# Kernel optimization log

Measured on AMD Instinct MI355X. Metric: run time of the kernel, lower is better.

## Reference

```python
import jax, jax.numpy as jnp
import numpy as np

INF = jnp.float32(1e9)


def _hungarian_min_perm(Cp, n):
    """Shortest-augmenting-path Hungarian (e-maxx variant) on padded cost Cp.
    Cp: (n+1, n+1) with Cp[i, j] = C[i-1, j-1] for i,j >= 1; row/col 0 virtual.
    Returns p: (n+1,) int32 where p[j] (j>=1) is the 1-based row assigned to col j.
    """
    cols = jnp.arange(n + 1)

    def outer(i, carry):
        u, v, p = carry
        p = p.at[0].set(i)
        init = (jnp.int32(0), u, v, p,
                jnp.full(n + 1, INF, Cp.dtype),
                jnp.zeros(n + 1, bool),
                jnp.zeros(n + 1, jnp.int32))

        def cond(s):
            j0, u, v, p, minv, used, way = s
            return p[j0] != 0

        def body(s):
            j0, u, v, p, minv, used, way = s
            used = used.at[j0].set(True)
            i0 = p[j0]
            cur = Cp[i0] - u[i0] - v                      # reduced costs, (n+1,)
            avail = (~used) & (cols >= 1)
            better = avail & (cur < minv)
            minv = jnp.where(better, cur, minv)
            way = jnp.where(better, j0, way)
            mv = jnp.where(avail, minv, INF)
            j1 = jnp.argmin(mv).astype(jnp.int32)
            delta = mv[j1]
            u = u.at[p].add(jnp.where(used, delta, 0.0))  # u[p[j]] += delta for used j
            v = v - jnp.where(used, delta, 0.0)
            minv = jnp.where(used, minv, minv - delta)
            return (j1, u, v, p, minv, used, way)

        j0, u, v, p, minv, used, way = jax.lax.while_loop(cond, body, init)

        # reconstruct augmenting path
        def cond2(s):
            return s[0] != 0

        def body2(s):
            j0, p = s
            j1 = way[j0]
            return (j1, p.at[j0].set(p[j1]))

        _, p = jax.lax.while_loop(cond2, body2, (j0, p))
        return (u, v, p)

    u0 = jnp.zeros(n + 1, Cp.dtype)
    v0 = jnp.zeros(n + 1, Cp.dtype)
    p0 = jnp.zeros(n + 1, jnp.int32)
    _, _, p = jax.lax.fori_loop(1, n + 1, outer, (u0, v0, p0))
    return p


def hungarian_maximize(a):
    """a: (n, n) benefit matrix -> (n, n) 0/1 optimal assignment matrix (maximize)."""
    n = a.shape[0]
    Cp = jnp.zeros((n + 1, n + 1), a.dtype).at[1:, 1:].set(-a)  # minimize -a
    p = _hungarian_min_perm(Cp, n)
    return jnp.zeros((n, n), jnp.float32).at[p[1:] - 1, jnp.arange(n)].set(1.0)


batched_lsa = jax.vmap(hungarian_maximize)


def setup_inputs() -> dict:
    key = jax.random.key(0)
    B, H, W = 1024, 128, 128
    x = jax.random.normal(key, (B, H, W), dtype=jnp.float32)
    bias = jnp.ones((H, W), dtype=jnp.float32)  # nn.Parameter(torch.ones(h, w))
    return {"x": x, "bias": bias}


def reference(x, bias):
    perm = batched_lsa(x)                               # (B, h, w) 0/1 assignments
    out = perm / jnp.sqrt(jnp.sum(perm * perm))         # global L2 norm (dim=None, keepdim)
    out = out * bias                                    # broadcast (h, w)
    return jax.nn.softmax(out, axis=2)                  # w >= h -> softmax over dim 2
```

## Files before the change

### kernel.cpp

```cpp
#include <hip/hip_runtime.h>
#include <hip/hip_fp16.h>

#define N 128
#define INF_ 1e9f
typedef unsigned long long ull;

__device__ __forceinline__ unsigned f2ord(float f) {
    unsigned b = __float_as_uint(f);
    return b ^ ((unsigned)((int)b >> 31) | 0x80000000u);
}
__device__ __forceinline__ float ord2f(unsigned k) {
    unsigned b = k ^ ((unsigned)((int)(~k) >> 31) | 0x80000000u);
    return __uint_as_float(b);
}
template <int CTRL>
__device__ __forceinline__ int dppmov(int v) {
    return __builtin_amdgcn_update_dpp(v, v, CTRL, 0xF, 0xF, false);
}
__device__ __forceinline__ int rl(int v, int lane) { return __builtin_amdgcn_readlane(v, lane); }
__device__ __forceinline__ unsigned uminu(unsigned a, unsigned b) { return a < b ? a : b; }

#define GMIN16(k) { \
    k = uminu(k, (unsigned)dppmov<0x121>((int)k)); \
    k = uminu(k, (unsigned)dppmov<0x122>((int)k)); \
    k = uminu(k, (unsigned)dppmov<0x124>((int)k)); \
    k = uminu(k, (unsigned)dppmov<0x128>((int)k)); \
}

__global__ void __launch_bounds__(64) lsa_solve_kernel(
        const float* __restrict__ x, const float* __restrict__ bias,
        float* __restrict__ out, int B) {
    __shared__ unsigned Cs[N][64];
    __shared__ float u_lds[N + 1];
    __shared__ int   p_lds[N + 1];
    __shared__ int   colOf[N + 1];
    __shared__ int   freeQ[N + 1];

    const int b = blockIdx.x;
    const int l = threadIdx.x;
    const int c0 = 2 * l + 1, c1 = 2 * l + 2;
    const ull mlt = (1ull << l) - 1;
    const float* xb = x + (size_t)b * (N * N);

    #pragma unroll 4
    for (int r = 0; r < N; ++r) {
        const float2 f = *(const float2*)&xb[r * N + 2 * l];
        __half2 h = __floats2half2_rn(-f.x, -f.y);
        Cs[r][l] = __builtin_bit_cast(unsigned, h);
    }
    u_lds[l] = 0.f;   u_lds[l + 64] = 0.f;
    p_lds[c0] = 0;    p_lds[c1] = 0;
    colOf[l + 1] = 0; colOf[l + 65] = 0;
    freeQ[l] = 0x7FFFFFFF; freeQ[l + 64] = 0x7FFFFFFF;
    if (l == 0) { u_lds[128] = 0.f; p_lds[0] = 0; colOf[0] = 0; freeQ[128] = 0x7FFFFFFF; }
    __syncthreads();

    float m0 = INF_, m1 = INF_; int am0 = 1, am1 = 1;
    #pragma unroll 4
    for (int r = 0; r < N; ++r) {
        __half2 h = __builtin_bit_cast(__half2, Cs[r][l]);
        float f0 = __low2float(h), f1 = __high2float(h);
        if (f0 < m0) { m0 = f0; am0 = r + 1; }
        if (f1 < m1) { m1 = f1; am1 = r + 1; }
    }
    float v0r = m0, v1r = m1;
    atomicMin(&freeQ[am0], c0);
    atomicMin(&freeQ[am1], c1);
    __syncthreads();
    int prow0 = (freeQ[am0] == c0) ? am0 : 0;
    int prow1 = (freeQ[am1] == c1) ? am1 : 0;
    p_lds[c0] = prow0;
    p_lds[c1] = prow1;
    if (prow0) colOf[am0] = c0;
    if (prow1) colOf[am1] = c1;
    __syncthreads();

    int nf;
    {
        int fA = (colOf[l + 1] == 0);
        int fB = (colOf[l + 65] == 0);
        ull bA = __ballot(fA), bB = __ballot(fB);
        int nA = __popcll(bA);
        if (fA) freeQ[__popcll(bA & mlt)] = l + 1;
        if (fB) freeQ[nA + __popcll(bB & mlt)] = l + 65;
        nf = nA + __popcll(bB);
    }
    __syncthreads();
    int qv0 = freeQ[l], qv1 = freeQ[l + 64];

    #pragma unroll 1
    for (int fi = 0; fi < nf; ++fi) {
        int sl = fi & 63;
        const int i = (fi < 64) ? rl(qv0, sl) : rl(qv1, sl);
        __half2 h = __builtin_bit_cast(__half2, Cs[i - 1][l]);
        float rc0 = __low2float(h)  - v0r;
        float rc1 = __high2float(h) - v1r;
        unsigned k0 = f2ord(rc0), k1 = f2ord(rc1);
        unsigned kl = uminu(k0, k1);
        int isHi = (k1 < k0) ? 1 : 0;
        unsigned kg = kl;
        GMIN16(kg)
        unsigned g0 = (unsigned)rl((int)kg, 0),  g1 = (unsigned)rl((int)kg, 16);
        unsigned g2 = (unsigned)rl((int)kg, 32), g3 = (unsigned)rl((int)kg, 48);
        unsigned gmin = uminu(uminu(g0, g1), uminu(g2, g3));
        ull bw = __ballot(kl == gmin);
        int wl = (int)__builtin_ctzll(bw);
        int hi = rl(isHi, wl);
        int jm = 2 * wl + 1 + hi;
        float mn = ord2f(gmin);
        if (l == 0) {
            u_lds[i] = mn;
            if (p_lds[jm] == 0) { p_lds[jm] = i; colOf[i] = jm; }
        }
    }
    __syncthreads();

    prow0 = p_lds[c0]; prow1 = p_lds[c1];
    float uprow0 = u_lds[prow0], uprow1 = u_lds[prow1];

    {
        int fA = (colOf[l + 1] == 0);
        int fB = (colOf[l + 65] == 0);
        ull bA = __ballot(fA), bB = __ballot(fB);
        int nA = __popcll(bA);
        if (fA) freeQ[__popcll(bA & mlt)] = l + 1;
        if (fB) freeQ[nA + __popcll(bB & mlt)] = l + 65;
        nf = nA + __popcll(bB);
    }
    __syncthreads();
    qv0 = freeQ[l]; qv1 = freeQ[l + 64];

    #pragma unroll 1
    for (int fi = 0; fi < nf; ++fi) {
        int sl = fi & 63;
        const int i = (fi < 64) ? rl(qv0, sl) : rl(qv1, sl);

        float dist0 = INF_, dist1 = INF_;
        int   way0 = 0, way1 = 0;
        float cumAt0 = 0.f, cumAt1 = 0.f;
        float cum = 0.f;
        float base = -u_lds[i];
        int   j0 = 0, i0 = i;

        #pragma unroll 1
        for (int it = 0; it <= N; ++it) {
            if (c0 == j0) { cumAt0 = cum; dist0 = __int_as_float(0x7FC00000); }
            if (c1 == j0) { cumAt1 = cum; dist1 = __int_as_float(0x7FC00000); }

            __half2 h = __builtin_bit_cast(__half2, Cs[i0 - 1][l]);
            float cand0 = __low2float(h)  - v0r + base;
            float cand1 = __high2float(h) - v1r + base;
            if (cand0 < dist0) { dist0 = cand0; way0 = j0; }
            if (cand1 < dist1) { dist1 = cand1; way1 = j0; }

            unsigned k0 = f2ord(dist0), k1 = f2ord(dist1);
            unsigned kl = uminu(k0, k1);
            int isHi = (k1 < k0) ? 1 : 0;
            unsigned kg = kl;
            GMIN16(kg)
            unsigned g0 = (unsigned)rl((int)kg, 0),  g1 = (unsigned)rl((int)kg, 16);
            unsigned g2 = (unsigned)rl((int)kg, 32), g3 = (unsigned)rl((int)kg, 48);
            unsigned gmin = uminu(uminu(g0, g1), uminu(g2, g3));
            ull bw = __ballot(kl == gmin);
            int wl = (int)__builtin_ctzll(bw);
            int hi = rl(isHi, wl);
            int pA = rl(prow0, wl), pB = rl(prow1, wl);
            int uA = rl(__float_as_int(uprow0), wl), uB = rl(__float_as_int(uprow1), wl);
            cum  = ord2f(gmin);
            j0   = 2 * wl + 1 + hi;
            i0   = hi ? pB : pA;
            base = cum - __int_as_float(hi ? uB : uA);
            if (i0 == 0) break;
        }

        bool used0 = (__float_as_uint(dist0) == 0x7FC00000u);
        bool used1 = (__float_as_uint(dist1) == 0x7FC00000u);
        if (used0) { float dv = cum - cumAt0; v0r -= dv; u_lds[prow0] += dv; }
        if (used1) { float dv = cum - cumAt1; v1r -= dv; u_lds[prow1] += dv; }
        if (l == 0) u_lds[i] += cum;
        __syncthreads();

        int j = j0;
        #pragma unroll 1
        while (j != 0) {
            int idx = j - 1, slw = idx >> 1, hib = idx & 1;
            int w0 = rl(way0, slw), w1 = rl(way1, slw);
            int jn = hib ? w1 : w0;
            int pn;
            if (jn == 0) pn = i;
            else {
                int pidx = jn - 1, slp = pidx >> 1, phb = pidx & 1;
                int p0 = rl(prow0, slp), p1 = rl(prow1, slp);
                pn = phb ? p1 : p0;
            }
            if (c0 == j) prow0 = pn;
            if (c1 == j) prow1 = pn;
            j = jn;
        }
        uprow0 = u_lds[prow0];
        uprow1 = u_lds[prow1];
    }

    colOf[prow0] = c0;
    colOf[prow1] = c1;
    __syncthreads();

    const float inv_norm = rsqrtf((float)B * (float)N);
    float* ob = out + (size_t)b * (N * N);
    #pragma unroll 2
    for (int r = 0; r < N; ++r) {
        int jA = __builtin_amdgcn_readfirstlane(colOf[r + 1]);
        float s = bias[r * N + (jA - 1)] * inv_norm;
        float e = __expf(s);
        float inv_d = 1.0f / (127.0f + e);
        float av = e * inv_d;
        float2 w;
        w.x = (c0 == jA) ? av : inv_d;
        w.y = (c1 == jA) ? av : inv_d;
        *(float2*)&ob[r * N + 2 * l] = w;
    }
}

extern "C" void kernel_launch(void* const* d_in, const int* in_sizes, int n_in,
                              void* d_out, int out_size, void* d_ws, size_t ws_size,
                              hipStream_t stream) {
    const float* x    = (const float*)d_in[0];
    const float* bias = (const float*)d_in[1];
    float* out = (float*)d_out;
    int B = in_sizes[0] / (N * N);
    hipLaunchKernelGGL(lsa_solve_kernel, dim3(B), dim3(64), 0, stream, x, bias, out, B);
}
```

Measured before the change: 325.0 us.

## Add reduction transfer and augmenting row reduction before Dijkstra phase

Adds the Jonker-Volgenant initialization steps: a reduction-transfer pass that lowers column duals of assigned columns by each row's second-best reduced cost, then two passes of augmenting row reduction that assign free rows greedily and may evict incumbents. It also moves the column-to-row map from shared memory into registers read via readlane. The goal is fewer free rows left for the expensive shortest-augmenting-path loop, at the cost of extra serial wave reductions during initialization.

```diff
diff --git a/kernel.cpp b/kernel.cpp
--- a/kernel.cpp
+++ b/kernel.cpp
@@ -18,6 +18,9 @@
     return __builtin_amdgcn_update_dpp(v, v, CTRL, 0xF, 0xF, false);
 }
 __device__ __forceinline__ int rl(int v, int lane) { return __builtin_amdgcn_readlane(v, lane); }
+__device__ __forceinline__ unsigned rlu(unsigned v, int lane) {
+    return (unsigned)__builtin_amdgcn_readlane((int)v, lane);
+}
 __device__ __forceinline__ unsigned uminu(unsigned a, unsigned b) { return a < b ? a : b; }
 
 #define GMIN16(k) { \
@@ -26,13 +29,16 @@
     k = uminu(k, (unsigned)dppmov<0x124>((int)k)); \
     k = uminu(k, (unsigned)dppmov<0x128>((int)k)); \
 }
+#define GMINALL(k, gmin) { \
+    unsigned _g0 = rlu(k, 0), _g1 = rlu(k, 16), _g2 = rlu(k, 32), _g3 = rlu(k, 48); \
+    gmin = uminu(uminu(_g0, _g1), uminu(_g2, _g3)); \
+}
 
 __global__ void __launch_bounds__(64) lsa_solve_kernel(
         const float* __restrict__ x, const float* __restrict__ bias,
         float* __restrict__ out, int B) {
     __shared__ unsigned Cs[N][64];
     __shared__ float u_lds[N + 1];
-    __shared__ int   p_lds[N + 1];
     __shared__ int   colOf[N + 1];
     __shared__ int   freeQ[N + 1];
 
@@ -49,10 +55,9 @@
         Cs[r][l] = __builtin_bit_cast(unsigned, h);
     }
     u_lds[l] = 0.f;   u_lds[l + 64] = 0.f;
-    p_lds[c0] = 0;    p_lds[c1] = 0;
     colOf[l + 1] = 0; colOf[l + 65] = 0;
     freeQ[l] = 0x7FFFFFFF; freeQ[l + 64] = 0x7FFFFFFF;
-    if (l == 0) { u_lds[128] = 0.f; p_lds[0] = 0; colOf[0] = 0; freeQ[128] = 0x7FFFFFFF; }
+    if (l == 0) { u_lds[128] = 0.f; colOf[0] = 0; freeQ[128] = 0x7FFFFFFF; }
     __syncthreads();
 
     float m0 = INF_, m1 = INF_; int am0 = 1, am1 = 1;
@@ -69,13 +74,98 @@
     __syncthreads();
     int prow0 = (freeQ[am0] == c0) ? am0 : 0;
     int prow1 = (freeQ[am1] == c1) ? am1 : 0;
-    p_lds[c0] = prow0;
-    p_lds[c1] = prow1;
     if (prow0) colOf[am0] = c0;
     if (prow1) colOf[am1] = c1;
     __syncthreads();
 
+    {
+        float pend0 = 0.f, pend1 = 0.f;
+        #pragma unroll 2
+        for (int r = 1; r <= N; ++r) {
+            int j1 = __builtin_amdgcn_readfirstlane(colOf[r]);
+            __half2 h = __builtin_bit_cast(__half2, Cs[r - 1][l]);
+            float rc0 = __low2float(h)  - v0r;
+            float rc1 = __high2float(h) - v1r;
+            if (c0 == j1) rc0 = INF_;
+            if (c1 == j1) rc1 = INF_;
+            unsigned k = uminu(f2ord(rc0), f2ord(rc1));
+            GMIN16(k)
+            unsigned gmin; GMINALL(k, gmin)
+            float m2 = ord2f(gmin);
+            if (j1 != 0) {
+                if (c0 == j1) pend0 = m2;
+                if (c1 == j1) pend1 = m2;
+            }
+        }
+        v0r -= pend0; v1r -= pend1;
+    }
+
     int nf;
+    {
+        int fA = (colOf[l + 1] == 0);
+        int fB = (colOf[l + 65] == 0);
+        ull bA = __ballot(fA), bB = __ballot(fB);
+        int nA = __popcll(bA);
+        if (fA) freeQ[__popcll(bA & mlt)] = l + 1;
+        if (fB) freeQ[nA + __popcll(bB & mlt)] = l + 65;
+        nf = nA + __popcll(bB);
+    }
+    __syncthreads();
+
+    {
+        int prv = nf;
+        #pragma unroll 1
+        for (int pass = 0; pass < 2 && prv > 0; ++pass) {
+            int wr = 0;
+            #pragma unroll 1
+            for (int kk = 0; kk < prv; ++kk) {
+                const int i = __builtin_amdgcn_readfirstlane(freeQ[kk]);
+                __half2 h = __builtin_bit_cast(__half2, Cs[i - 1][l]);
+                float rc0 = __low2float(h)  - v0r;
+                float rc1 = __high2float(h) - v1r;
+                unsigned k0 = f2ord(rc0), k1 = f2ord(rc1);
+                unsigned klmin = uminu(k0, k1);
+                int isHi = (k1 < k0) ? 1 : 0;
+                unsigned kg = klmin;
+                GMIN16(kg)
+                unsigned gmin; GMINALL(kg, gmin)
+                ull bw = __ballot(klmin == gmin);
+                int wl = (int)__builtin_ctzll(bw);
+                int hi1 = rl(isHi, wl);
+                int j1 = 2 * wl + 1 + hi1;
+                unsigned oth = (l == wl) ? (hi1 ? k0 : k1) : klmin;
+                unsigned kg2 = oth;
+                GMIN16(kg2)
+                unsigned m2o; GMINALL(kg2, m2o)
+                if (gmin < m2o) {
+                    float d = ord2f(m2o) - ord2f(gmin);
+                    if (c0 == j1) v0r -= d;
+                    if (c1 == j1) v1r -= d;
+                } else {
+                    int sl1 = (j1 - 1) >> 1;
+                    int pj1 = ((j1 - 1) & 1) ? rl(prow1, sl1) : rl(prow0, sl1);
+                    if (pj1 != 0) {
+                        ull bw2 = __ballot(oth == m2o);
+                        int wl2 = (int)__builtin_ctzll(bw2);
+                        int hi2 = (wl2 == wl) ? (hi1 ^ 1) : rl(isHi, wl2);
+                        j1 = 2 * wl2 + 1 + hi2;
+                    }
+                }
+                int slj = (j1 - 1) >> 1;
+                int inc = ((j1 - 1) & 1) ? rl(prow1, slj) : rl(prow0, slj);
+                if (c0 == j1) prow0 = i;
+                if (c1 == j1) prow1 = i;
+                if (l == 0) {
+                    colOf[i] = j1;
+                    if (inc != 0) { colOf[inc] = 0; freeQ[wr] = inc; }
+                }
+                if (inc != 0) ++wr;
+            }
+            prv = wr;
+            __syncthreads();
+        }
+    }
+
     {
         int fA = (colOf[l + 1] == 0);
         int fB = (colOf[l + 65] == 0);
@@ -100,23 +190,31 @@
         int isHi = (k1 < k0) ? 1 : 0;
         unsigned kg = kl;
         GMIN16(kg)
-        unsigned g0 = (unsigned)rl((int)kg, 0),  g1 = (unsigned)rl((int)kg, 16);
-        unsigned g2 = (unsigned)rl((int)kg, 32), g3 = (unsigned)rl((int)kg, 48);
-        unsigned gmin = uminu(uminu(g0, g1), uminu(g2, g3));
+        unsigned gmin; GMINALL(kg, gmin)
         ull bw = __ballot(kl == gmin);
         int wl = (int)__builtin_ctzll(bw);
         int hi = rl(isHi, wl);
         int jm = 2 * wl + 1 + hi;
-        float mn = ord2f(gmin);
-        if (l == 0) {
-            u_lds[i] = mn;
-            if (p_lds[jm] == 0) { p_lds[jm] = i; colOf[i] = jm; }
-        }
-    }
-    __syncthreads();
-
-    prow0 = p_lds[c0]; prow1 = p_lds[c1];
-    float uprow0 = u_lds[prow0], uprow1 = u_lds[prow1];
+        if (l == 0) u_lds[i] = ord2f(gmin);
+        int slm = (jm - 1) >> 1;
+        int pm = ((jm - 1) & 1) ? rl(prow1, slm) : rl(prow0, slm);
+        if (pm == 0) {
+            if (c0 == jm) prow0 = i;
+            if (c1 == jm) prow1 = i;
+            if (l == 0) colOf[i] = jm;
+        }
+    }
+    __syncthreads();
+
+    if (prow0) {
+        __half2 h = __builtin_bit_cast(__half2, Cs[prow0 - 1][l]);
+        u_lds[prow0] = __low2float(h) - v0r;
+    }
+    if (prow1) {
+        __half2 h = __builtin_bit_cast(__half2, Cs[prow1 - 1][l]);
+        u_lds[prow1] = __high2float(h) - v1r;
+    }
+    __syncthreads();
 
     {
         int fA = (colOf[l + 1] == 0);
@@ -129,6 +227,7 @@
     }
     __syncthreads();
     qv0 = freeQ[l]; qv1 = freeQ[l + 64];
+    float uprow0 = u_lds[prow0], uprow1 = u_lds[prow1];
 
     #pragma unroll 1
     for (int fi = 0; fi < nf; ++fi) {
@@ -158,9 +257,7 @@
             int isHi = (k1 < k0) ? 1 : 0;
             unsigned kg = kl;
             GMIN16(kg)
-            unsigned g0 = (unsigned)rl((int)kg, 0),  g1 = (unsigned)rl((int)kg, 16);
-            unsigned g2 = (unsigned)rl((int)kg, 32), g3 = (unsigned)rl((int)kg, 48);
-            unsigned gmin = uminu(uminu(g0, g1), uminu(g2, g3));
+            unsigned gmin; GMINALL(kg, gmin)
             ull bw = __ballot(kl == gmin);
             int wl = (int)__builtin_ctzll(bw);
             int hi = rl(isHi, wl);
```

After: 308.8 us. 5.0% less time.
